# Kernel tuning notes

Hardware: AMD Instinct MI355X
Metric: run time of the kernel (lower is better)

Reference implementation:

```python
import jax, jax.numpy as jnp
import numpy as np

B, T, D, E, H, K = 4, 2048, 1024, 8, 2048, 2


def setup_inputs() -> dict:
    key = jax.random.key(0)
    k0, k1, k2, k3 = jax.random.split(key, 4)
    x = jax.random.normal(k0, (B, T, D), dtype=jnp.float32)
    router_w = jax.random.normal(k1, (E, D), dtype=jnp.float32) * (D ** -0.5)
    w1 = jax.random.normal(k2, (E, D, H), dtype=jnp.float32) * (D ** -0.5)
    w2 = jax.random.normal(k3, (E, H, D), dtype=jnp.float32) * (H ** -0.5)
    return {"x": x, "router_w": router_w, "w1": w1, "w2": w2}


def reference(x, router_w, w1, w2):
    Bb, Tt, Dd = x.shape
    N = Bb * Tt
    # --- router: top-k selection + renormalized softmax weights ---
    logits = jnp.einsum('btd,ed->bte', x, router_w)            # [B,T,E]
    top_vals, top_idx = jax.lax.top_k(logits, K)               # [B,T,K]
    top_w = jax.nn.softmax(top_vals, axis=-1)                  # [B,T,K]
    # --- dense per-expert FFN (relu-squared activation) ---
    xf = x.reshape(N, Dd)                                      # [N,D]
    h = jnp.einsum('nd,edh->enh', xf, w1)                      # [E,N,H]
    h = jnp.square(jax.nn.relu(h))
    y = jnp.einsum('enh,ehd->end', h, w2)                      # [E,N,D]
    # --- gather selected experts and combine ---
    idx_f = top_idx.reshape(N, K)                              # [N,K]
    w_f = top_w.reshape(N, K)                                  # [N,K]
    y_sel = y[idx_f, jnp.arange(N)[:, None]]                   # [N,K,D]
    out = jnp.einsum('nk,nkd->nd', w_f, y_sel)                 # [N,D]
    return out.reshape(Bb, Tt, Dd)
```

## Files before the change

kernel.cpp:

```cpp
#include <hip/hip_runtime.h>
#include <hip/hip_bf16.h>
#include <stdint.h>

#define ND    1024
#define NE    8
#define NH    2048
#define NTOK  8192
#define NPAIR (NTOK*2)

typedef unsigned short u16;
typedef __attribute__((ext_vector_type(8))) short bf16x8;
typedef __attribute__((ext_vector_type(4))) float f32x4;

__device__ __forceinline__ u16 f2bf(float f) {
    union { float f; unsigned u; } v; v.f = f;
    return (u16)((v.u + 0x7fffu + ((v.u >> 16) & 1u)) >> 16);
}

__device__ __forceinline__ void gl_lds16(const void* g, void* l) {
    __builtin_amdgcn_global_load_lds(
        (const __attribute__((address_space(1))) unsigned int*)g,
        (__attribute__((address_space(3))) unsigned int*)l, 16, 0, 0);
}

#define CTRL_OFFS  16
#define CTRL_BC    32
#define CTRL_BB    288
#define CTRL_TOPK  544

__global__ __launch_bounds__(256) void router_topk2(
    const float* __restrict__ x, const float* __restrict__ rw,
    int* __restrict__ topk_idx, float* __restrict__ topk_w)
{
    const int n    = blockIdx.x * 4 + (threadIdx.x >> 6);
    const int lane = threadIdx.x & 63;
    const float* xr = x + (size_t)n * ND;
    float4 xv[4];
    #pragma unroll
    for (int i = 0; i < 4; ++i) xv[i] = *(const float4*)(xr + lane*16 + i*4);

    float lg[NE];
    #pragma unroll
    for (int e = 0; e < NE; ++e) {
        const float* wr_ = rw + (size_t)e * ND + lane*16;
        float a = 0.f;
        #pragma unroll
        for (int i = 0; i < 4; ++i) {
            float4 wv = *(const float4*)(wr_ + i*4);
            a += xv[i].x*wv.x + xv[i].y*wv.y + xv[i].z*wv.z + xv[i].w*wv.w;
        }
        #pragma unroll
        for (int s = 32; s; s >>= 1) a += __shfl_xor(a, s);
        lg[e] = a;
    }
    if (lane == 0) {
        int i0 = 0; float v0 = lg[0];
        #pragma unroll
        for (int i = 1; i < NE; ++i) { float v = lg[i]; if (v > v0) { v0 = v; i0 = i; } }
        int i1 = -1; float v1 = -3.4e38f;
        #pragma unroll
        for (int i = 0; i < NE; ++i) {
            if (i == i0) continue;
            float v = lg[i]; if (v > v1) { v1 = v; i1 = i; }
        }
        float w0 = 1.f / (1.f + expf(v1 - v0));
        topk_idx[n*2]   = i0;  topk_idx[n*2+1] = i1;
        topk_w [n*2]    = w0;  topk_w [n*2+1]  = 1.f - w0;
    }
}

__global__ __launch_bounds__(256) void hist_blocks(
    const int* __restrict__ topk_idx, int* __restrict__ blockcounts)
{
    __shared__ int c[NE];
    const int tid = threadIdx.x;
    if (tid < NE) c[tid] = 0;
    __syncthreads();
    const int n = blockIdx.x * 256 + tid;
    atomicAdd(&c[topk_idx[n*2]],   1);
    atomicAdd(&c[topk_idx[n*2+1]], 1);
    __syncthreads();
    if (tid < NE) blockcounts[blockIdx.x * NE + tid] = c[tid];
}

__global__ void prefix2(int* __restrict__ ctrl)
{
    const int e = threadIdx.x;
    const int* bc = ctrl + CTRL_BC;
    int* offsets  = ctrl + CTRL_OFFS;
    int* bbase    = ctrl + CTRL_BB;
    if (e < NE) {
        int run = 0;
        int tmp[32];
        #pragma unroll
        for (int b = 0; b < 32; ++b) { tmp[b] = run; run += bc[b*NE + e]; }
        int total = run, pre = 0;
        #pragma unroll
        for (int i = 0; i < NE; ++i) {
            int v = __shfl(total, i);
            if (i < e) pre += v;
        }
        offsets[e] = pre;
        if (e == NE-1) offsets[NE] = pre + total;
        #pragma unroll
        for (int b = 0; b < 32; ++b) bbase[b*NE + e] = pre + tmp[b];
    }
}

__global__ __launch_bounds__(256) void scatter2(
    const int* __restrict__ topk_idx, const float* __restrict__ topk_w,
    const int* __restrict__ ctrl,
    int* __restrict__ bucket_tok, float* __restrict__ bucket_gw)
{
    __shared__ int wc[4][NE];
    const int b = blockIdx.x, tid = threadIdx.x;
    const int w = tid >> 6, l = tid & 63;
    const int n = b*256 + tid;
    const int e0 = topk_idx[n*2], e1 = topk_idx[n*2+1];
    const unsigned long long lt = (1ULL << l) - 1ULL;

    int rank0 = 0, rank1 = 0;
    #pragma unroll
    for (int e = 0; e < NE; ++e) {
        unsigned long long m0 = __ballot(e0 == e);
        unsigned long long m1 = __ballot(e1 == e);
        int c0 = __popcll(m0);
        if (e0 == e) rank0 = __popcll(m0 & lt);
        if (e1 == e) rank1 = c0 + __popcll(m1 & lt);
        if (l == 0) wc[w][e] = c0 + __popcll(m1);
    }
    __syncthreads();
    const int* bbase = ctrl + CTRL_BB;
    int wo0 = 0, wo1 = 0;
    #pragma unroll
    for (int w2 = 0; w2 < 4; ++w2) {
        if (w2 < w) { wo0 += wc[w2][e0]; wo1 += wc[w2][e1]; }
    }
    int p0 = bbase[b*NE + e0] + wo0 + rank0;
    int p1 = bbase[b*NE + e1] + wo1 + rank1;
    bucket_tok[p0] = n;  bucket_gw[p0] = topk_w[n*2];
    bucket_tok[p1] = n;  bucket_gw[p1] = topk_w[n*2+1];
}

__global__ __launch_bounds__(256) void transpose_cvt(
    const float* __restrict__ src, u16* __restrict__ dst, int R, int C)
{
    __shared__ float tb[64][65];
    const int tpc = C >> 6;
    const int tr = blockIdx.x / tpc;
    const int tc = blockIdx.x % tpc;
    src += (size_t)blockIdx.y * R * C;
    dst += (size_t)blockIdx.y * R * C;
    const int tid = threadIdx.x;
    #pragma unroll
    for (int i = 0; i < 4; ++i) {
        int idx = i*256 + tid;
        int r = idx >> 4, c4 = (idx & 15) * 4;
        float4 v = *(const float4*)(src + (size_t)(tr*64 + r)*C + tc*64 + c4);
        tb[r][c4] = v.x; tb[r][c4+1] = v.y; tb[r][c4+2] = v.z; tb[r][c4+3] = v.w;
    }
    __syncthreads();
    #pragma unroll
    for (int i = 0; i < 2; ++i) {
        int idx = i*256 + tid;
        int c = idx >> 3, s8 = (idx & 7) * 8;
        union { u16 u[8]; uint4 v; } pk;
        #pragma unroll
        for (int j = 0; j < 8; ++j) pk.u[j] = f2bf(tb[s8 + j][c]);
        *(uint4*)(dst + (size_t)(tc*64 + c)*R + tr*64 + s8) = pk.v;
    }
}

__global__ __launch_bounds__(256) void gather_cvt(
    const float* __restrict__ x, const int* __restrict__ bucket_tok, u16* __restrict__ Xg)
{
    const int pair = blockIdx.x * 4 + (threadIdx.x >> 6);
    const int lane = threadIdx.x & 63;
    const float* xr = x + (size_t)bucket_tok[pair] * ND;
    u16* dr = Xg + (size_t)pair * ND;
    const int d0 = lane * 16;
    float4 a = *(const float4*)(xr + d0);
    float4 b = *(const float4*)(xr + d0 + 4);
    float4 c = *(const float4*)(xr + d0 + 8);
    float4 d = *(const float4*)(xr + d0 + 12);
    union { u16 u[8]; uint4 v; } p0, p1;
    p0.u[0]=f2bf(a.x); p0.u[1]=f2bf(a.y); p0.u[2]=f2bf(a.z); p0.u[3]=f2bf(a.w);
    p0.u[4]=f2bf(b.x); p0.u[5]=f2bf(b.y); p0.u[6]=f2bf(b.z); p0.u[7]=f2bf(b.w);
    p1.u[0]=f2bf(c.x); p1.u[1]=f2bf(c.y); p1.u[2]=f2bf(c.z); p1.u[3]=f2bf(c.w);
    p1.u[4]=f2bf(d.x); p1.u[5]=f2bf(d.y); p1.u[6]=f2bf(d.z); p1.u[7]=f2bf(d.w);
    *(uint4*)(dr + d0)     = p0.v;
    *(uint4*)(dr + d0 + 8) = p1.v;
}

template<int KSTEPS, int EPI>
__global__ __launch_bounds__(512, 2) void pass_gemm(
    const u16* __restrict__ Amat, const u16* __restrict__ Bmat,
    const int* __restrict__ bucket_tok, const float* __restrict__ bucket_gw,
    const int* __restrict__ ctrl,
    u16* __restrict__ A1out, float* __restrict__ out)
{
    const int K   = KSTEPS * 64;
    const int e   = blockIdx.z;
    const int nt0 = blockIdx.x * 256;
    const int mt0 = blockIdx.y * 256;
    const int* offsets = ctrl + CTRL_OFFS;
    const int beg = offsets[e];
    const int cnt = offsets[e+1] - beg;
    if (mt0 >= cnt) return;

    extern __shared__ u16 sm[];

    const int tid  = threadIdx.x;
    const int wv   = tid >> 6;
    const int lane = tid & 63;
    const int l15  = lane & 15;
    const int grp  = lane >> 4;
    const int wr   = wv >> 2;
    const int wc   = wv & 3;
    const int rmax = cnt - mt0 - 1;

    const u16* Abase = Amat + (size_t)beg * K;
    const u16* Bb    = Bmat + (size_t)e * NH * ND;

    const int rsub8 = lane >> 3;
    const int cs    = lane & 7;

    auto stage = [&](int buf, int kt) {
        #pragma unroll
        for (int c = 0; c < 4; ++c) {
            int row   = wv*32 + c*8 + rsub8;
            int chunk = cs ^ (row & 7);
            int lrow  = row > rmax ? rmax : row;
            const u16* ga = Abase + (size_t)(mt0 + lrow) * K + kt*64 + chunk*8;
            gl_lds16(ga, sm + buf*16384 + wv*2048 + c*512);
            const u16* gb = Bb + (size_t)(nt0 + row) * K + kt*64 + chunk*8;
            gl_lds16(gb, sm + 32768 + buf*16384 + wv*2048 + c*512);
        }
    };

    f32x4 acc[8][4];
    #pragma unroll
    for (int mt = 0; mt < 8; ++mt)
        #pragma unroll
        for (int nt = 0; nt < 4; ++nt) acc[mt][nt] = 0;

    stage(0, 0);
    int cur = 0;
    for (int kt = 0; kt < KSTEPS; ++kt) {
        __syncthreads();
        if (kt + 1 < KSTEPS) stage(cur ^ 1, kt + 1);
        const char* As = (const char*)(sm + cur*16384);
        const char* Bs = (const char*)(sm + 32768 + cur*16384);
        #pragma unroll
        for (int kk = 0; kk < 2; ++kk) {
            bf16x8 bfr[4];
            #pragma unroll
            for (int nt = 0; nt < 4; ++nt) {
                int row = wc*64 + nt*16 + l15;
                int kb  = ((kk*4 + grp) ^ (row & 7)) << 4;
                bfr[nt] = *(const bf16x8*)(Bs + row*128 + kb);
            }
            #pragma unroll
            for (int mt = 0; mt < 8; ++mt) {
                int row = wr*128 + mt*16 + l15;
                int kb  = ((kk*4 + grp) ^ (row & 7)) << 4;
                bf16x8 af = *(const bf16x8*)(As + row*128 + kb);
                #pragma unroll
                for (int nt = 0; nt < 4; ++nt)
                    acc[mt][nt] = __builtin_amdgcn_mfma_f32_16x16x32_bf16(af, bfr[nt], acc[mt][nt], 0,0,0);
            }
        }
        cur ^= 1;
    }

    #pragma unroll
    for (int mt = 0; mt < 8; ++mt) {
        #pragma unroll
        for (int r = 0; r < 4; ++r) {
            int ml = mt0 + wr*128 + mt*16 + grp*4 + r;
            if (ml >= cnt) continue;
            if (EPI == 0) {
                u16* dst = A1out + (size_t)(beg + ml) * NH + nt0 + wc*64 + l15;
                #pragma unroll
                for (int nt = 0; nt < 4; ++nt) {
                    float v = fmaxf(acc[mt][nt][r], 0.f);
                    dst[nt*16] = f2bf(v * v);
                }
            } else {
                int   p = bucket_tok[beg + ml];
                float g = bucket_gw [beg + ml];
                float* orow = out + (size_t)p * ND + nt0 + wc*64 + l15;
                #pragma unroll
                for (int nt = 0; nt < 4; ++nt)
                    atomicAdd(orow + nt*16, g * acc[mt][nt][r]);
            }
        }
    }
}

extern "C" void kernel_launch(void* const* d_in, const int* in_sizes, int n_in,
                              void* d_out, int out_size, void* d_ws, size_t ws_size,
                              hipStream_t stream) {
    const float* x  = (const float*)d_in[0];
    const float* rw = (const float*)d_in[1];
    const float* w1 = (const float*)d_in[2];
    const float* w2 = (const float*)d_in[3];
    float* out = (float*)d_out;

    int*   ctrl        = (int*)d_ws;
    int*   blockcounts = ctrl + CTRL_BC;
    int*   topk_idx    = ctrl + CTRL_TOPK;
    float* topk_w      = (float*)(topk_idx + NPAIR);
    int*   bucket_tok  = (int*)(topk_w + NPAIR);
    float* bucket_gw   = (float*)(bucket_tok + NPAIR);

    const size_t CTRL_BYTES = (size_t)1 << 19;
    const size_t WT_BYTES   = (size_t)NE * NH * ND * sizeof(u16);
    const size_t A1_BYTES   = (size_t)NPAIR * NH * sizeof(u16);

    hipMemsetAsync(d_out, 0, (size_t)NTOK * ND * sizeof(float), stream);

    router_topk2<<<NTOK/4, 256, 0, stream>>>(x, rw, topk_idx, topk_w);
    hist_blocks<<<NTOK/256, 256, 0, stream>>>(topk_idx, blockcounts);
    prefix2<<<1, 64, 0, stream>>>(ctrl);
    scatter2<<<NTOK/256, 256, 0, stream>>>(topk_idx, topk_w, ctrl, bucket_tok, bucket_gw);

    u16* w1t = (u16*)((char*)d_ws + CTRL_BYTES);
    u16* shr = (u16*)((char*)d_ws + CTRL_BYTES + WT_BYTES);
    u16* A1  = (u16*)((char*)d_ws + CTRL_BYTES + 2*WT_BYTES);

    transpose_cvt<<<dim3(512, NE), 256, 0, stream>>>(w1, w1t, ND, NH);
    gather_cvt<<<NPAIR/4, 256, 0, stream>>>(x, bucket_tok, shr);

    pass_gemm<16, 0><<<dim3(NH/256, NPAIR/256, NE), 512, 131072, stream>>>(
        shr, w1t, bucket_tok, bucket_gw, ctrl, A1, nullptr);

    transpose_cvt<<<dim3(512, NE), 256, 0, stream>>>(w2, shr, NH, ND);

    pass_gemm<32, 1><<<dim3(ND/256, NPAIR/256, NE), 512, 131072, stream>>>(
        A1, shr, bucket_tok, bucket_gw, ctrl, nullptr, out);
}
```

Measured before the change: 324.3 us.

## Shrink grouped GEMM tiles to 128x128 with 4 waves and interleave experts over a flat grid

Both grouped GEMM passes now use 128x128 output tiles with 256 threads and half the LDS, instead of 256x256 tiles with 512 threads. A flat 1D grid maps block IDs so consecutive blocks land on different experts. The aim is more, smaller blocks that fill the GPU better and waste less work on partial tiles for experts with uneven token counts. The cost is lower arithmetic intensity per tile and more global/L2 traffic to re-read A and B, plus a larger worst-case grid with many blocks that exit early.

After: 290.1 us. 10.5% less time.

```diff
diff --git a/kernel.cpp b/kernel.cpp
--- a/kernel.cpp
+++ b/kernel.cpp
@@ -192,17 +192,20 @@
     *(uint4*)(dr + d0 + 8) = p1.v;
 }
 
-template<int KSTEPS, int EPI>
-__global__ __launch_bounds__(512, 2) void pass_gemm(
+template<int KSTEPS, int EPI, int NT_TILES, int WPE_SHIFT>
+__global__ __launch_bounds__(256, 2) void pass_gemm(
     const u16* __restrict__ Amat, const u16* __restrict__ Bmat,
     const int* __restrict__ bucket_tok, const float* __restrict__ bucket_gw,
     const int* __restrict__ ctrl,
     u16* __restrict__ A1out, float* __restrict__ out)
 {
     const int K   = KSTEPS * 64;
-    const int e   = blockIdx.z;
-    const int nt0 = blockIdx.x * 256;
-    const int mt0 = blockIdx.y * 256;
+    const int bid = blockIdx.x;
+    const int w   = ((bid & 7) << WPE_SHIFT) | (bid >> 3);
+    const int e   = w >> WPE_SHIFT;
+    const int r   = w & ((1 << WPE_SHIFT) - 1);
+    const int nt0 = (r % NT_TILES) * 128;
+    const int mt0 = (r / NT_TILES) * 128;
     const int* offsets = ctrl + CTRL_OFFS;
     const int beg = offsets[e];
     const int cnt = offsets[e+1] - beg;
@@ -215,32 +218,31 @@
     const int lane = tid & 63;
     const int l15  = lane & 15;
     const int grp  = lane >> 4;
-    const int wr   = wv >> 2;
-    const int wc   = wv & 3;
+    const int wr   = wv >> 1, wc = wv & 1;
     const int rmax = cnt - mt0 - 1;
 
     const u16* Abase = Amat + (size_t)beg * K;
     const u16* Bb    = Bmat + (size_t)e * NH * ND;
 
-    const int rsub8 = lane >> 3;
-    const int cs    = lane & 7;
+    const int rsub  = lane >> 3;
+    const int csrc0 = lane & 7;
 
     auto stage = [&](int buf, int kt) {
         #pragma unroll
         for (int c = 0; c < 4; ++c) {
-            int row   = wv*32 + c*8 + rsub8;
-            int chunk = cs ^ (row & 7);
-            int lrow  = row > rmax ? rmax : row;
+            int row = c*32 + wv*8 + rsub;
+            int chunk = csrc0 ^ (row & 7);
+            int lrow = row > rmax ? rmax : row;
             const u16* ga = Abase + (size_t)(mt0 + lrow) * K + kt*64 + chunk*8;
-            gl_lds16(ga, sm + buf*16384 + wv*2048 + c*512);
+            gl_lds16(ga, sm + buf*8192 + c*2048 + wv*512);
             const u16* gb = Bb + (size_t)(nt0 + row) * K + kt*64 + chunk*8;
-            gl_lds16(gb, sm + 32768 + buf*16384 + wv*2048 + c*512);
+            gl_lds16(gb, sm + 16384 + buf*8192 + c*2048 + wv*512);
         }
     };
 
-    f32x4 acc[8][4];
-    #pragma unroll
-    for (int mt = 0; mt < 8; ++mt)
+    f32x4 acc[4][4];
+    #pragma unroll
+    for (int mt = 0; mt < 4; ++mt)
         #pragma unroll
         for (int nt = 0; nt < 4; ++nt) acc[mt][nt] = 0;
 
@@ -249,41 +251,43 @@
     for (int kt = 0; kt < KSTEPS; ++kt) {
         __syncthreads();
         if (kt + 1 < KSTEPS) stage(cur ^ 1, kt + 1);
-        const char* As = (const char*)(sm + cur*16384);
-        const char* Bs = (const char*)(sm + 32768 + cur*16384);
+        const char* As = (const char*)(sm + cur*8192);
+        const char* Bs = (const char*)(sm + 16384 + cur*8192);
         #pragma unroll
         for (int kk = 0; kk < 2; ++kk) {
-            bf16x8 bfr[4];
+            bf16x8 af[4], bfr[4];
+            #pragma unroll
+            for (int mt = 0; mt < 4; ++mt) {
+                int row = wr*64 + mt*16 + l15;
+                int kb  = ((kk*32 + grp*8)*2) ^ ((row & 7) << 4);
+                af[mt] = *(const bf16x8*)(As + row*128 + kb);
+            }
             #pragma unroll
             for (int nt = 0; nt < 4; ++nt) {
                 int row = wc*64 + nt*16 + l15;
-                int kb  = ((kk*4 + grp) ^ (row & 7)) << 4;
+                int kb  = ((kk*32 + grp*8)*2) ^ ((row & 7) << 4);
                 bfr[nt] = *(const bf16x8*)(Bs + row*128 + kb);
             }
             #pragma unroll
-            for (int mt = 0; mt < 8; ++mt) {
-                int row = wr*128 + mt*16 + l15;
-                int kb  = ((kk*4 + grp) ^ (row & 7)) << 4;
-                bf16x8 af = *(const bf16x8*)(As + row*128 + kb);
+            for (int mt = 0; mt < 4; ++mt)
                 #pragma unroll
                 for (int nt = 0; nt < 4; ++nt)
-                    acc[mt][nt] = __builtin_amdgcn_mfma_f32_16x16x32_bf16(af, bfr[nt], acc[mt][nt], 0,0,0);
-            }
+                    acc[mt][nt] = __builtin_amdgcn_mfma_f32_16x16x32_bf16(af[mt], bfr[nt], acc[mt][nt], 0,0,0);
         }
         cur ^= 1;
     }
 
     #pragma unroll
-    for (int mt = 0; mt < 8; ++mt) {
-        #pragma unroll
-        for (int r = 0; r < 4; ++r) {
-            int ml = mt0 + wr*128 + mt*16 + grp*4 + r;
+    for (int mt = 0; mt < 4; ++mt) {
+        #pragma unroll
+        for (int r4 = 0; r4 < 4; ++r4) {
+            int ml = mt0 + wr*64 + mt*16 + grp*4 + r4;
             if (ml >= cnt) continue;
             if (EPI == 0) {
                 u16* dst = A1out + (size_t)(beg + ml) * NH + nt0 + wc*64 + l15;
                 #pragma unroll
                 for (int nt = 0; nt < 4; ++nt) {
-                    float v = fmaxf(acc[mt][nt][r], 0.f);
+                    float v = fmaxf(acc[mt][nt][r4], 0.f);
                     dst[nt*16] = f2bf(v * v);
                 }
             } else {
@@ -292,7 +296,7 @@
                 float* orow = out + (size_t)p * ND + nt0 + wc*64 + l15;
                 #pragma unroll
                 for (int nt = 0; nt < 4; ++nt)
-                    atomicAdd(orow + nt*16, g * acc[mt][nt][r]);
+                    atomicAdd(orow + nt*16, g * acc[mt][nt][r4]);
             }
         }
     }
@@ -316,7 +320,6 @@
 
     const size_t CTRL_BYTES = (size_t)1 << 19;
     const size_t WT_BYTES   = (size_t)NE * NH * ND * sizeof(u16);
-    const size_t A1_BYTES   = (size_t)NPAIR * NH * sizeof(u16);
 
     hipMemsetAsync(d_out, 0, (size_t)NTOK * ND * sizeof(float), stream);
 
@@ -332,11 +335,11 @@
     transpose_cvt<<<dim3(512, NE), 256, 0, stream>>>(w1, w1t, ND, NH);
     gather_cvt<<<NPAIR/4, 256, 0, stream>>>(x, bucket_tok, shr);
 
-    pass_gemm<16, 0><<<dim3(NH/256, NPAIR/256, NE), 512, 131072, stream>>>(
+    pass_gemm<16, 0, 16, 11><<<8 << 11, 256, 65536, stream>>>(
         shr, w1t, bucket_tok, bucket_gw, ctrl, A1, nullptr);
 
     transpose_cvt<<<dim3(512, NE), 256, 0, stream>>>(w2, shr, NH, ND);
 
-    pass_gemm<32, 1><<<dim3(ND/256, NPAIR/256, NE), 512, 131072, stream>>>(
+    pass_gemm<32, 1, 8, 10><<<8 << 10, 256, 65536, stream>>>(
         A1, shr, bucket_tok, bucket_gw, ctrl, nullptr, out);
 }
```
